# Kernel optimization log

Measured on AMD Instinct MI355X. Metric: run time of the kernel, lower is better.

Reference implementation:

```python
import jax, jax.numpy as jnp
import numpy as np

B, T = 64, 512
OBS, DM, DS, NL = 115, 128, 8, 3
EMB, NA, H1 = 16, 19, 256


def _ln(x, g, b, eps=1e-5):
    m = jnp.mean(x, -1, keepdims=True)
    v = jnp.mean((x - m) ** 2, -1, keepdims=True)
    return (x - m) * jax.lax.rsqrt(v + eps) * g + b


def _s6(x, h, lng, lnb, w_ig, w_dt, b_dt, a_log, w_b, w_c, d_par, w_out):
    # x: [B,T,DM], h: [B,DM,DS]
    xn = _ln(x, lng, lnb)
    xp = xn @ w_ig.T                               # [B,T,2*DM]
    x_in, z = xp[..., :DM], xp[..., DM:]
    dt = jax.nn.softplus(x_in @ w_dt.T + b_dt)     # [B,T,DM]
    A = -jnp.exp(a_log)                            # [DM,DS]
    bt = x_in @ w_b.T                              # [B,T,DS]
    ct = x_in @ w_c.T                              # [B,T,DS]
    dA = jnp.exp(dt[..., None] * A)                # [B,T,DM,DS]
    upd = (dt * x_in)[..., None] * bt[:, :, None, :]  # [B,T,DM,DS]

    def step(hc, inp):
        dA_t, u_t, c_t = inp
        hn = dA_t * hc + u_t                       # [B,DM,DS]
        y = jnp.einsum('bds,bs->bd', hn, c_t)      # [B,DM]
        return hn, y

    h_f, ys = jax.lax.scan(
        step, h,
        (jnp.swapaxes(dA, 0, 1), jnp.swapaxes(upd, 0, 1), jnp.swapaxes(ct, 0, 1)))
    y = jnp.swapaxes(ys, 0, 1)                     # [B,T,DM]
    ssm = y * jax.nn.silu(z) + x_in * d_par
    return x + ssm @ w_out.T, h_f.reshape(h_f.shape[0], -1)


def _forward(prev_actions, obs, h0, enc_w1, enc_b1, enc_g1, enc_bb1, enc_w2, enc_b2,
             enc_g2, enc_bb2, emb, proj_w, proj_b, proj_g, proj_bb,
             m_ln_g, m_ln_b, m_w_ig, m_w_dt, m_b_dt, m_a_log, m_w_b, m_w_c, m_d, m_w_out,
             fn_g, fn_b, pol_w1, pol_b1, pol_g, pol_bb, pol_w2, pol_b2):
    # MLP encoder: Linear -> LN -> SiLU -> Linear -> LN (final norm)
    e = jax.nn.silu(_ln(obs @ enc_w1.T + enc_b1, enc_g1, enc_bb1))
    e = _ln(e @ enc_w2.T + enc_b2, enc_g2, enc_bb2)
    pa = emb[prev_actions]                         # [B,T,EMB]
    x = jnp.concatenate([e, pa], -1) @ proj_w.T + proj_b
    x = jax.nn.silu(_ln(x, proj_g, proj_bb))
    for i in range(NL):
        x, _ = _s6(x, h0[i].reshape(-1, DM, DS), m_ln_g[i], m_ln_b[i], m_w_ig[i],
                   m_w_dt[i], m_b_dt[i], m_a_log[i], m_w_b[i], m_w_c[i], m_d[i], m_w_out[i])
    x = _ln(x, fn_g, fn_b)
    p = jax.nn.silu(_ln(x @ pol_w1.T + pol_b1, pol_g, pol_bb))
    return p @ pol_w2.T + pol_b2                   # [B,T,NA] policy logits


def setup_inputs() -> dict:
    key = jax.random.key(0)
    ks = iter(jax.random.split(key, 64))
    def n(shape, s=0.05):
        return jax.random.normal(next(ks), shape, dtype=jnp.float32) * s
    return {
        'obs': jax.random.normal(next(ks), (B, T, OBS), dtype=jnp.float32),
        'h0': jnp.zeros((NL, B, DM * DS), jnp.float32),
        'enc_w1': n((H1, OBS)), 'enc_b1': jnp.zeros((H1,)),
        'enc_g1': jnp.ones((H1,)), 'enc_bb1': jnp.zeros((H1,)),
        'enc_w2': n((DM, H1)), 'enc_b2': jnp.zeros((DM,)),
        'enc_g2': jnp.ones((DM,)), 'enc_bb2': jnp.zeros((DM,)),
        'emb': n((NA + 1, EMB), 1.0),
        'proj_w': n((DM, DM + EMB)), 'proj_b': jnp.zeros((DM,)),
        'proj_g': jnp.ones((DM,)), 'proj_bb': jnp.zeros((DM,)),
        'm_ln_g': jnp.ones((NL, DM)), 'm_ln_b': jnp.zeros((NL, DM)),
        'm_w_ig': n((NL, 2 * DM, DM)), 'm_w_dt': n((NL, DM, DM)),
        'm_b_dt': jnp.zeros((NL, DM)),
        'm_a_log': jax.random.uniform(next(ks), (NL, DM, DS), minval=-3.0, maxval=-1.0, dtype=jnp.float32),
        'm_w_b': n((NL, DS, DM)), 'm_w_c': n((NL, DS, DM)),
        'm_d': jnp.ones((NL, DM)), 'm_w_out': n((NL, DM, DM)),
        'fn_g': jnp.ones((DM,)), 'fn_b': jnp.zeros((DM,)),
        'pol_w1': n((DM, DM)), 'pol_b1': jnp.zeros((DM,)),
        'pol_g': jnp.ones((DM,)), 'pol_bb': jnp.zeros((DM,)),
        'pol_w2': n((NA, DM)), 'pol_b2': jnp.zeros((NA,)),
        'prev_actions': jax.random.randint(next(ks), (B, T), 0, NA + 1),
    }


def reference(obs, h0, enc_w1, enc_b1, enc_g1, enc_bb1, enc_w2, enc_b2, enc_g2, enc_bb2,
              emb, proj_w, proj_b, proj_g, proj_bb, m_ln_g, m_ln_b, m_w_ig, m_w_dt,
              m_b_dt, m_a_log, m_w_b, m_w_c, m_d, m_w_out, fn_g, fn_b, pol_w1, pol_b1,
              pol_g, pol_bb, pol_w2, pol_b2, prev_actions):
    return _forward(prev_actions, obs, h0, enc_w1, enc_b1, enc_g1, enc_bb1, enc_w2,
                    enc_b2, enc_g2, enc_bb2, emb, proj_w, proj_b, proj_g, proj_bb,
                    m_ln_g, m_ln_b, m_w_ig, m_w_dt, m_b_dt, m_a_log, m_w_b, m_w_c,
                    m_d, m_w_out, fn_g, fn_b, pol_w1, pol_b1, pol_g, pol_bb, pol_w2, pol_b2)
```

## Files before the change

### kernel.cpp

```cpp
#include <hip/hip_runtime.h>
#include <math.h>

#define BB 64
#define TT 512
#define OBSD 115
#define DMD 128
#define DSD 8
#define NLD 3
#define EMBD 16
#define NAD 19
#define H1D 256
#define NTOK (BB*TT)
#define SSEG 32
#define TSEG (TT/SSEG)

typedef unsigned short ushort_t;
typedef __attribute__((ext_vector_type(8))) short short8;
typedef __attribute__((ext_vector_type(4))) float f32x4;

__device__ __forceinline__ float silu_f(float x){ return x / (1.f + __expf(-x)); }
__device__ __forceinline__ float softplus_f(float x){
  return fmaxf(x, 0.f) + log1pf(__expf(-fabsf(x)));
}
__device__ __forceinline__ ushort_t f2bf(float x){
  unsigned u = __float_as_uint(x);
  unsigned r = (u + 0x7fffu + ((u >> 16) & 1u)) >> 16;
  return (ushort_t)r;
}
__device__ __forceinline__ float b2f(ushort_t x){
  return __uint_as_float(((unsigned)x) << 16);
}
#define MFMA(a,b,c) __builtin_amdgcn_mfma_f32_16x16x32_bf16((a),(b),(c),0,0,0)
#define LOG2E 1.44269504f

struct PJob { const float* src; ushort_t* dst; int N; int K; int Kpad; int rowofs; int Nw; };
struct PJobs { PJob j[20]; };

__global__ __launch_bounds__(256) void k_prep(PJobs P){
  const int job = blockIdx.x >> 2;
  const int sub = blockIdx.x & 3;
  PJob pj = P.j[job];
  const int elems = pj.Nw * pj.Kpad;
  for (int idx = sub*256 + threadIdx.x; idx < elems; idx += 4*256){
    int n = idx / pj.Kpad;
    int k = idx - n*pj.Kpad;
    float v = (n < pj.N && k < pj.K) ? pj.src[(size_t)n*pj.K + k] : 0.f;
    pj.dst[(size_t)(pj.rowofs + n)*pj.Kpad + k] = f2bf(v);
  }
}

__global__ __launch_bounds__(256, 4) void k_enc12p(
    const float* __restrict__ obs, const ushort_t* __restrict__ w1b,
    const float* __restrict__ b1, const float* __restrict__ g1,
    const float* __restrict__ bb1,
    const ushort_t* __restrict__ w2b,
    const float* __restrict__ b2, const float* __restrict__ g2,
    const float* __restrict__ bb2,
    const float* __restrict__ emb, const int* __restrict__ pact,
    const ushort_t* __restrict__ pwb, const float* __restrict__ pb,
    const float* __restrict__ pg, const float* __restrict__ pbb,
    float* __restrict__ X,
    const float* __restrict__ lng, const float* __restrict__ lnb,
    const ushort_t* __restrict__ wigb, const ushort_t* __restrict__ wdbcb,
    const float* __restrict__ bdt,
    ushort_t* __restrict__ XINb, ushort_t* __restrict__ Zb,
    ushort_t* __restrict__ DTb, ushort_t* __restrict__ BTu, ushort_t* __restrict__ CTu,
    const float* __restrict__ alog0,
    float* __restrict__ HLOC, float* __restrict__ PPR)
{
  __shared__ __align__(16) char sm[29184];
  ushort_t* s_obs  = (ushort_t*)sm;
  ushort_t* s_e1   = (ushort_t*)sm;
  ushort_t* s_xin  = (ushort_t*)sm;
  ushort_t* s_dt   = (ushort_t*)(sm + 8704);
  ushort_t* s_a2   = (ushort_t*)(sm + 16896);
  ushort_t* s_btc  = (ushort_t*)(sm + 27648);
  float2*   s_st   = (float2*)(sm + 28160);
  float2*   s_st2  = (float2*)(sm + 28672);

  const int tok0 = blockIdx.x * 32;
  const int bidx = blockIdx.x >> 4;
  const int ch   = blockIdx.x & 15;
  const int tid = threadIdx.x;
  const int lane = tid & 63, w = tid >> 6;
  const int q = lane >> 4, cn = lane & 15;
  const int m0 = (w & 1) * 16, nh = w >> 1;

  for (int e = tid; e < 32*16; e += 256){
    int t = e >> 4, kc = e & 15;
    const float* op = obs + (size_t)(tok0 + t)*OBSD;
    short8 v;
    #pragma unroll
    for (int j = 0; j < 8; j++){
      int k = kc*8 + j;
      v[j] = (short)f2bf(k < OBSD ? op[k] : 0.f);
    }
    *(short8*)&s_obs[t*136 + kc*8] = v;
  }
  for (int e = tid; e < 32*32; e += 256){
    int t = e >> 5, k = e & 31;
    float v = 0.f;
    if (k < EMBD){ int a = pact[tok0 + t]; v = emb[(size_t)a*EMBD + k]; }
    s_a2[t*168 + 128 + k] = f2bf(v);
  }
  __syncthreads();

  f32x4 acc[8];
  {
    short8 af[4];
    #pragma unroll
    for (int ks = 0; ks < 4; ks++)
      af[ks] = *(const short8*)&s_obs[(m0 + cn)*136 + ks*32 + q*8];
    #pragma unroll
    for (int nt = 0; nt < 8; nt++){
      const int n0 = (nh*8 + nt) * 16;
      f32x4 a = {0.f,0.f,0.f,0.f};
      #pragma unroll
      for (int ks = 0; ks < 4; ks++){
        short8 bf = *(const short8*)&w1b[(size_t)(n0 + cn)*128 + ks*32 + q*8];
        a = MFMA(af[ks], bf, a);
      }
      float bv = b1[n0 + cn];
      #pragma unroll
      for (int r = 0; r < 4; r++) a[r] += bv;
      acc[nt] = a;
    }
    #pragma unroll
    for (int r = 0; r < 4; r++){
      float s = 0.f, s2 = 0.f;
      #pragma unroll
      for (int nt = 0; nt < 8; nt++){ float v = acc[nt][r]; s += v; s2 = fmaf(v, v, s2); }
      s += __shfl_xor(s, 1, 64); s2 += __shfl_xor(s2, 1, 64);
      s += __shfl_xor(s, 2, 64); s2 += __shfl_xor(s2, 2, 64);
      s += __shfl_xor(s, 4, 64); s2 += __shfl_xor(s2, 4, 64);
      s += __shfl_xor(s, 8, 64); s2 += __shfl_xor(s2, 8, 64);
      if (cn == 0) s_st[(m0 + q*4 + r)*2 + nh] = make_float2(s, s2);
    }
  }
  __syncthreads();

  {
    float mu[4], rs[4];
    #pragma unroll
    for (int r = 0; r < 4; r++){
      const int row = m0 + q*4 + r;
      float2 p0 = s_st[row*2 + 0], p1 = s_st[row*2 + 1];
      float s = p0.x + p1.x, s2 = p0.y + p1.y;
      float m = s * (1.f/256.f);
      mu[r] = m;
      rs[r] = rsqrtf(s2 * (1.f/256.f) - m*m + 1e-5f);
    }
    #pragma unroll
    for (int nt = 0; nt < 8; nt++){
      const int col = (nh*8 + nt)*16 + cn;
      float gg = g1[col], bbv = bb1[col];
      #pragma unroll
      for (int r = 0; r < 4; r++){
        float v = (acc[nt][r] - mu[r]) * rs[r] * gg + bbv;
        s_e1[(m0 + q*4 + r)*264 + col] = f2bf(silu_f(v));
      }
    }
  }
  __syncthreads();

  f32x4 acc2[4];
  {
    short8 af2[8];
    #pragma unroll
    for (int ks = 0; ks < 8; ks++)
      af2[ks] = *(const short8*)&s_e1[(m0 + cn)*264 + ks*32 + q*8];
    #pragma unroll
    for (int nt = 0; nt < 4; nt++){
      const int n0 = (nh*4 + nt) * 16;
      f32x4 a = {0.f,0.f,0.f,0.f};
      #pragma unroll
      for (int ks = 0; ks < 8; ks++){
        short8 bf = *(const short8*)&w2b[(size_t)(n0 + cn)*256 + ks*32 + q*8];
        a = MFMA(af2[ks], bf, a);
      }
      float bv = b2[n0 + cn];
      #pragma unroll
      for (int r = 0; r < 4; r++) a[r] += bv;
      acc2[nt] = a;
    }
    #pragma unroll
    for (int r = 0; r < 4; r++){
      float s = 0.f, s2 = 0.f;
      #pragma unroll
      for (int nt = 0; nt < 4; nt++){ float v = acc2[nt][r]; s += v; s2 = fmaf(v, v, s2); }
      s += __shfl_xor(s, 1, 64); s2 += __shfl_xor(s2, 1, 64);
      s += __shfl_xor(s, 2, 64); s2 += __shfl_xor(s2, 2, 64);
      s += __shfl_xor(s, 4, 64); s2 += __shfl_xor(s2, 4, 64);
      s += __shfl_xor(s, 8, 64); s2 += __shfl_xor(s2, 8, 64);
      if (cn == 0) s_st[(m0 + q*4 + r)*2 + nh] = make_float2(s, s2);
    }
  }
  __syncthreads();

  {
    float mu[4], rs[4];
    #pragma unroll
    for (int r = 0; r < 4; r++){
      const int row = m0 + q*4 + r;
      float2 p0 = s_st[row*2 + 0], p1 = s_st[row*2 + 1];
      float s = p0.x + p1.x, s2 = p0.y + p1.y;
      float m = s * (1.f/128.f);
      mu[r] = m;
      rs[r] = rsqrtf(s2 * (1.f/128.f) - m*m + 1e-5f);
    }
    #pragma unroll
    for (int nt = 0; nt < 4; nt++){
      const int col = (nh*4 + nt)*16 + cn;
      float gg = g2[col], bbv = bb2[col];
      #pragma unroll
      for (int r = 0; r < 4; r++){
        float v = (acc2[nt][r] - mu[r]) * rs[r] * gg + bbv;
        s_a2[(m0 + q*4 + r)*168 + col] = f2bf(v);
      }
    }
  }
  __syncthreads();

  f32x4 acc3[4];
  {
    short8 af3[5];
    #pragma unroll
    for (int ks = 0; ks < 5; ks++)
      af3[ks] = *(const short8*)&s_a2[(m0 + cn)*168 + ks*32 + q*8];
    #pragma unroll
    for (int nt = 0; nt < 4; nt++){
      const int n0 = (nh*4 + nt) * 16;
      f32x4 a = {0.f,0.f,0.f,0.f};
      #pragma unroll
      for (int ks = 0; ks < 5; ks++){
        short8 bf = *(const short8*)&pwb[(size_t)(n0 + cn)*160 + ks*32 + q*8];
        a = MFMA(af3[ks], bf, a);
      }
      float bv = pb[n0 + cn];
      #pragma unroll
      for (int r = 0; r < 4; r++) a[r] += bv;
      acc3[nt] = a;
    }
    #pragma unroll
    for (int r = 0; r < 4; r++){
      float s = 0.f, s2 = 0.f;
      #pragma unroll
      for (int nt = 0; nt < 4; nt++){ float v = acc3[nt][r]; s += v; s2 = fmaf(v, v, s2); }
      s += __shfl_xor(s, 1, 64); s2 += __shfl_xor(s2, 1, 64);
      s += __shfl_xor(s, 2, 64); s2 += __shfl_xor(s2, 2, 64);
      s += __shfl_xor(s, 4, 64); s2 += __shfl_xor(s2, 4, 64);
      s += __shfl_xor(s, 8, 64); s2 += __shfl_xor(s2, 8, 64);
      if (cn == 0) s_st[(m0 + q*4 + r)*2 + nh] = make_float2(s, s2);
    }
  }
  __syncthreads();

  {
    float mu[4], rs[4];
    #pragma unroll
    for (int r = 0; r < 4; r++){
      const int row = m0 + q*4 + r;
      float2 p0 = s_st[row*2 + 0], p1 = s_st[row*2 + 1];
      float s = p0.x + p1.x, s2 = p0.y + p1.y;
      float m = s * (1.f/128.f);
      mu[r] = m;
      rs[r] = rsqrtf(s2 * (1.f/128.f) - m*m + 1e-5f);
    }
    float ps[4] = {0.f,0.f,0.f,0.f}, ps2[4] = {0.f,0.f,0.f,0.f};
    #pragma unroll
    for (int nt = 0; nt < 4; nt++){
      const int col = (nh*4 + nt)*16 + cn;
      float gg = pg[col], bbv = pbb[col];
      #pragma unroll
      for (int r = 0; r < 4; r++){
        float v = (acc3[nt][r] - mu[r]) * rs[r] * gg + bbv;
        v = silu_f(v);
        acc3[nt][r] = v;
        X[(size_t)(tok0 + m0 + q*4 + r)*128 + col] = v;
        ps[r] += v; ps2[r] = fmaf(v, v, ps2[r]);
      }
    }
    #pragma unroll
    for (int r = 0; r < 4; r++){
      float s = ps[r], s2 = ps2[r];
      s += __shfl_xor(s, 1, 64); s2 += __shfl_xor(s2, 1, 64);
      s += __shfl_xor(s, 2, 64); s2 += __shfl_xor(s2, 2, 64);
      s += __shfl_xor(s, 4, 64); s2 += __shfl_xor(s2, 4, 64);
      s += __shfl_xor(s, 8, 64); s2 += __shfl_xor(s2, 8, 64);
      if (cn == 0) s_st2[(m0 + q*4 + r)*2 + nh] = make_float2(s, s2);
    }
  }
  __syncthreads();

  {
    float mu[4], rs[4];
    #pragma unroll
    for (int r = 0; r < 4; r++){
      const int row = m0 + q*4 + r;
      float2 p0 = s_st2[row*2 + 0], p1 = s_st2[row*2 + 1];
      float s = p0.x + p1.x, s2 = p0.y + p1.y;
      float m = s * (1.f/128.f);
      mu[r] = m;
      rs[r] = rsqrtf(s2 * (1.f/128.f) - m*m + 1e-5f);
    }
    #pragma unroll
    for (int nt = 0; nt < 4; nt++){
      const int col = (nh*4 + nt)*16 + cn;
      float gg = lng[col], bbv = lnb[col];
      #pragma unroll
      for (int r = 0; r < 4; r++){
        float v = (acc3[nt][r] - mu[r]) * rs[r] * gg + bbv;
        s_a2[(m0 + q*4 + r)*168 + col] = f2bf(v);
      }
    }
  }
  __syncthreads();

  {
    short8 af[4];
    #pragma unroll
    for (int ks = 0; ks < 4; ks++)
      af[ks] = *(const short8*)&s_a2[(m0 + cn)*168 + ks*32 + q*8];
    #pragma unroll
    for (int nt = 0; nt < 8; nt++){
      const int n0 = (nh*8 + nt) * 16;
      f32x4 a = {0.f,0.f,0.f,0.f};
      #pragma unroll
      for (int ks = 0; ks < 4; ks++){
        short8 bf = *(const short8*)&wigb[(size_t)(n0 + cn)*128 + ks*32 + q*8];
        a = MFMA(af[ks], bf, a);
      }
      if (n0 < 128){
        #pragma unroll
        for (int r = 0; r < 4; r++){
          int tr = m0 + q*4 + r;
          ushort_t bb = f2bf(a[r]);
          XINb[(size_t)(tok0 + tr)*128 + n0 + cn] = bb;
          s_xin[tr*136 + n0 + cn] = bb;
        }
      } else {
        #pragma unroll
        for (int r = 0; r < 4; r++){
          int tr = m0 + q*4 + r;
          Zb[(size_t)(tok0 + tr)*128 + (n0 - 128) + cn] = f2bf(a[r]);
        }
      }
    }
  }
  __syncthreads();

  {
    short8 af2[4];
    #pragma unroll
    for (int ks = 0; ks < 4; ks++)
      af2[ks] = *(const short8*)&s_xin[(m0 + cn)*136 + ks*32 + q*8];
    for (int nt = nh; nt < 9; nt += 2){
      const int n0 = nt * 16;
      f32x4 a = {0.f,0.f,0.f,0.f};
      #pragma unroll
      for (int ks = 0; ks < 4; ks++){
        short8 bf = *(const short8*)&wdbcb[(size_t)(n0 + cn)*128 + ks*32 + q*8];
        a = MFMA(af2[ks], bf, a);
      }
      const int col = n0 + cn;
      if (col < 128){
        float bd = bdt[col];
        #pragma unroll
        for (int r = 0; r < 4; r++){
          int tr = m0 + q*4 + r;
          ushort_t dv = f2bf(softplus_f(a[r] + bd));
          DTb[(size_t)(tok0 + tr)*128 + col] = dv;
          s_dt[tr*136 + col] = dv;
        }
      } else if (col < 136){
        #pragma unroll
        for (int r = 0; r < 4; r++){
          int tr = m0 + q*4 + r;
          ushort_t bb = f2bf(a[r]);
          BTu[(size_t)(tok0 + tr)*8 + (col - 128)] = bb;
          s_btc[tr*8 + (col - 128)] = bb;
        }
      } else {
        #pragma unroll
        for (int r = 0; r < 4; r++)
          CTu[(size_t)(tok0 + m0 + q*4 + r)*8 + (col - 136)] = f2bf(a[r]);
      }
    }
  }
  __syncthreads();

  {
    const int d = tid & 127, half = tid >> 7;
    float A2c[8], hh[8], pp[8];
    #pragma unroll
    for (int s = 0; s < 8; s++){
      A2c[s] = -__expf(alog0[d*8 + s]) * LOG2E;
      hh[s] = 0.f; pp[s] = 1.f;
    }
    const int t0 = half * 16;
    #pragma unroll 4
    for (int tt = 0; tt < 16; tt++){
      const int t = t0 + tt;
      float dt = b2f(s_dt[t*136 + d]);
      float wv = dt * b2f(s_xin[t*136 + d]);
      #pragma unroll
      for (int s = 0; s < 8; s++){
        float dA = exp2f(dt * A2c[s]);
        hh[s] = fmaf(dA, hh[s], wv * b2f(s_btc[t*8 + s]));
        pp[s] *= dA;
      }
    }
    const size_t o = ((size_t)bidx*SSEG + ch*2 + half)*1024 + d*8;
    #pragma unroll
    for (int s = 0; s < 8; s++){ HLOC[o+s] = hh[s]; PPR[o+s] = pp[s]; }
  }
}

__global__ __launch_bounds__(256) void k_carry(
    float* __restrict__ HL, const float* __restrict__ PP,
    const float* __restrict__ h0g)
{
  const int idx = blockIdx.x*256 + threadIdx.x;
  const size_t base = (size_t)(idx >> 10) * (SSEG*1024) + (idx & 1023);
  float hl[SSEG], pp[SSEG];
  #pragma unroll
  for (int ch = 0; ch < SSEG; ch++){
    hl[ch] = HL[base + (size_t)ch*1024];
    pp[ch] = PP[base + (size_t)ch*1024];
  }
  float h = h0g[idx];
  #pragma unroll
  for (int ch = 0; ch < SSEG; ch++){
    HL[base + (size_t)ch*1024] = h;
    h = fmaf(pp[ch], h, hl[ch]);
  }
}

#define SMB 34816

__device__ __forceinline__ void phaseB32(
    const ushort_t* DTb, const ushort_t* XINb, const ushort_t* Zb,
    const ushort_t* BTu, const ushort_t* CTu,
    const float* __restrict__ alog, const float* __restrict__ HLpre,
    const float* __restrict__ dpar, const ushort_t* __restrict__ woutb,
    float* __restrict__ X, char* sm, int b, int pair, int tid)
{
  ushort_t* s_dtS = (ushort_t*)sm;
  ushort_t* s_xiS = (ushort_t*)(sm + 8192);
  ushort_t* s_zS  = (ushort_t*)(sm + 16384);
  float*    s_x   = (float*)sm;
  ushort_t* s_a   = (ushort_t*)(sm + 24576);
  ushort_t* s_bt  = (ushort_t*)(sm + 33280);
  ushort_t* s_ct  = (ushort_t*)(sm + 33792);
  float2*   s_st  = (float2*)(sm + 34304);

  const int lane = tid & 63, w = tid >> 6, q = lane >> 4, cn = lane & 15;
  const int m0 = (w & 1) * 16, nh = w >> 1;
  const int d = tid & 127, half = tid >> 7;
  const size_t segtok = (size_t)b*TT + pair*32;

  {
    const uint4* gdt = (const uint4*)(DTb + segtok*128);
    const uint4* gxi = (const uint4*)(XINb + segtok*128);
    const uint4* gz  = (const uint4*)(Zb + segtok*128);
    #pragma unroll
    for (int i = 0; i < 2; i++){
      ((uint4*)s_dtS)[tid + i*256] = gdt[tid + i*256];
      ((uint4*)s_xiS)[tid + i*256] = gxi[tid + i*256];
      ((uint4*)s_zS )[tid + i*256] = gz [tid + i*256];
    }
    if (tid < 128){
      ((unsigned*)s_bt)[tid] = ((const unsigned*)(BTu + segtok*8))[tid];
      ((unsigned*)s_ct)[tid] = ((const unsigned*)(CTu + segtok*8))[tid];
    }
  }
  float A2[8], h[8];
  float dp = dpar[d];
  {
    const size_t o = ((size_t)b*SSEG + pair*2 + half)*1024 + d*8;
    float4 h0v = *(const float4*)(HLpre + o);
    float4 h1v = *(const float4*)(HLpre + o + 4);
    h[0]=h0v.x; h[1]=h0v.y; h[2]=h0v.z; h[3]=h0v.w;
    h[4]=h1v.x; h[5]=h1v.y; h[6]=h1v.z; h[7]=h1v.w;
    #pragma unroll
    for (int s = 0; s < 8; s++) A2[s] = -__expf(alog[d*8 + s]) * LOG2E;
  }
  __syncthreads();

  #pragma unroll 4
  for (int tt = 0; tt < 16; tt++){
    const int t = half*16 + tt;
    float dt = b2f(s_dtS[t*128 + d]);
    float xi = b2f(s_xiS[t*128 + d]);
    float zv = b2f(s_zS [t*128 + d]);
    float wv = dt * xi;
    float y = 0.f;
    #pragma unroll
    for (int s = 0; s < 8; s++){
      float dA = exp2f(dt * A2[s]);
      h[s] = fmaf(dA, h[s], wv * b2f(s_bt[t*8 + s]));
      y = fmaf(h[s], b2f(s_ct[t*8 + s]), y);
    }
    float ssm = y * silu_f(zv) + xi * dp;
    s_a[t*136 + d] = f2bf(ssm);
  }
  __syncthreads();

  {
    short8 af[4];
    #pragma unroll
    for (int ks = 0; ks < 4; ks++)
      af[ks] = *(const short8*)&s_a[(m0 + cn)*136 + ks*32 + q*8];
    float ps[4] = {0.f,0.f,0.f,0.f}, ps2[4] = {0.f,0.f,0.f,0.f};
    #pragma unroll
    for (int i = 0; i < 4; i++){
      const int n0 = (nh*4 + i) * 16;
      short8 bf[4];
      #pragma unroll
      for (int ks = 0; ks < 4; ks++)
        bf[ks] = *(const short8*)&woutb[(size_t)(n0+cn)*128 + ks*32 + q*8];
      f32x4 acc = {0.f,0.f,0.f,0.f};
      #pragma unroll
      for (int ks = 0; ks < 4; ks++) acc = MFMA(af[ks], bf[ks], acc);
      #pragma unroll
      for (int r = 0; r < 4; r++){
        const int tr = m0 + q*4 + r;
        const size_t g = (segtok + tr)*128 + n0 + cn;
        float xn = X[g] + acc[r];
        X[g] = xn;
        s_x[tr*130 + n0 + cn] = xn;
        ps[r] += xn; ps2[r] = fmaf(xn, xn, ps2[r]);
      }
    }
    #pragma unroll
    for (int r = 0; r < 4; r++){
      float s = ps[r], s2 = ps2[r];
      s += __shfl_xor(s, 1, 64); s2 += __shfl_xor(s2, 1, 64);
      s += __shfl_xor(s, 2, 64); s2 += __shfl_xor(s2, 2, 64);
      s += __shfl_xor(s, 4, 64); s2 += __shfl_xor(s2, 4, 64);
      s += __shfl_xor(s, 8, 64); s2 += __shfl_xor(s2, 8, 64);
      if (cn == 0) s_st[(m0 + q*4 + r)*2 + nh] = make_float2(s, s2);
    }
  }
  __syncthreads();
}

__global__ __launch_bounds__(256, 4) void k_scan2p(
    ushort_t* DTb, ushort_t* XINb, ushort_t* Zb,
    ushort_t* BTu, ushort_t* CTu,
    const float* __restrict__ alog, const float* __restrict__ HLpre,
    const float* __restrict__ dpar, const ushort_t* __restrict__ woutb,
    float* __restrict__ X,
    const float* __restrict__ lng, const float* __restrict__ lnb,
    const ushort_t* __restrict__ wigb, const ushort_t* __restrict__ wdbcb,
    const float* __restrict__ bdt,
    const float* __restrict__ alogn,
    float* __restrict__ HLo, float* __restrict__ PPo)
{
  __shared__ __align__(16) char sm[SMB];
  const int tid = threadIdx.x;
  float*    s_x   = (float*)sm;
  ushort_t* s_xin = (ushort_t*)sm;
  ushort_t* s_dt2 = (ushort_t*)(sm + 8704);
  ushort_t* s_a   = (ushort_t*)(sm + 24576);
  ushort_t* s_btc = (ushort_t*)(sm + 33280);
  float2*   s_st  = (float2*)(sm + 34304);

  const int b = blockIdx.x >> 4;
  const int pair = blockIdx.x & 15;
  const int lane = tid & 63, w = tid >> 6, q = lane >> 4, cn = lane & 15;
  const int m0 = (w & 1) * 16, nh = w >> 1;
  const int d = tid & 127, half = tid >> 7;
  const size_t segtok = (size_t)b*TT + pair*32;

  phaseB32(DTb, XINb, Zb, BTu, CTu, alog, HLpre, dpar, woutb, X, sm, b, pair, tid);

  {
    float g = lng[d], c0v = lnb[d];
    #pragma unroll
    for (int tt = 0; tt < 16; tt++){
      const int t = half*16 + tt;
      float2 p0 = s_st[t*2 + 0], p1 = s_st[t*2 + 1];
      float ssum = p0.x + p1.x, ss2 = p0.y + p1.y;
      float mu = ssum * (1.f/128.f);
      float rs = rsqrtf(ss2 * (1.f/128.f) - mu*mu + 1e-5f);
      float v = (s_x[t*130 + d] - mu) * rs * g + c0v;
      s_a[t*136 + d] = f2bf(v);
    }
  }
  __syncthreads();

  {
    short8 af[4];
    #pragma unroll
    for (int ks = 0; ks < 4; ks++)
      af[ks] = *(const short8*)&s_a[(m0 + cn)*136 + ks*32 + q*8];
    #pragma unroll
    for (int i = 0; i < 8; i++){
      const int n0 = (nh*8 + i) * 16;
      short8 bf[4];
      #pragma unroll
      for (int ks = 0; ks < 4; ks++)
        bf[ks] = *(const short8*)&wigb[(size_t)(n0+cn)*128 + ks*32 + q*8];
      f32x4 acc = {0.f,0.f,0.f,0.f};
      #pragma unroll
      for (int ks = 0; ks < 4; ks++) acc = MFMA(af[ks], bf[ks], acc);
      if (n0 < 128){
        #pragma unroll
        for (int r = 0; r < 4; r++){
          const int tr = m0 + q*4 + r;
          ushort_t bb = f2bf(acc[r]);
          XINb[(segtok + tr)*128 + n0 + cn] = bb;
          s_xin[tr*136 + n0 + cn] = bb;
        }
      } else {
        #pragma unroll
        for (int r = 0; r < 4; r++){
          const int tr = m0 + q*4 + r;
          Zb[(segtok + tr)*128 + (n0-128) + cn] = f2bf(acc[r]);
        }
      }
    }
  }
  __syncthreads();

  {
    short8 af2[4];
    #pragma unroll
    for (int ks = 0; ks < 4; ks++)
      af2[ks] = *(const short8*)&s_xin[(m0 + cn)*136 + ks*32 + q*8];
    for (int nt = nh; nt < 9; nt += 2){
      const int n0 = nt * 16;
      short8 bf[4];
      #pragma unroll
      for (int ks = 0; ks < 4; ks++)
        bf[ks] = *(const short8*)&wdbcb[(size_t)(n0+cn)*128 + ks*32 + q*8];
      f32x4 acc = {0.f,0.f,0.f,0.f};
      #pragma unroll
      for (int ks = 0; ks < 4; ks++) acc = MFMA(af2[ks], bf[ks], acc);
      const int col = n0 + cn;
      if (col < 128){
        float bd = bdt[col];
        #pragma unroll
        for (int r = 0; r < 4; r++){
          const int tr = m0 + q*4 + r;
          ushort_t dv = f2bf(softplus_f(acc[r] + bd));
          DTb[(segtok + tr)*128 + col] = dv;
          s_dt2[tr*136 + col] = dv;
        }
      } else if (col < 136){
        #pragma unroll
        for (int r = 0; r < 4; r++){
          const int tr = m0 + q*4 + r;
          ushort_t bb = f2bf(acc[r]);
          BTu[(segtok + tr)*8 + (col-128)] = bb;
          s_btc[tr*8 + (col-128)] = bb;
        }
      } else {
        #pragma unroll
        for (int r = 0; r < 4; r++)
          CTu[(segtok + m0 + q*4 + r)*8 + (col-136)] = f2bf(acc[r]);
      }
    }
  }
  __syncthreads();

  {
    float A2n[8], hh[8], pp[8];
    #pragma unroll
    for (int s = 0; s < 8; s++){
      A2n[s] = -__expf(alogn[d*8 + s]) * LOG2E;
      hh[s] = 0.f; pp[s] = 1.f;
    }
    #pragma unroll 4
    for (int tt = 0; tt < 16; tt++){
      const int t = half*16 + tt;
      float dt = b2f(s_dt2[t*136 + d]);
      float wv = dt * b2f(s_xin[t*136 + d]);
      #pragma unroll
      for (int s = 0; s < 8; s++){
        float dA = exp2f(dt * A2n[s]);
        hh[s] = fmaf(dA, hh[s], wv * b2f(s_btc[t*8 + s]));
        pp[s] *= dA;
      }
    }
    const size_t o = ((size_t)b*SSEG + pair*2 + half)*1024 + d*8;
    #pragma unroll
    for (int s = 0; s < 8; s++){ HLo[o+s] = hh[s]; PPo[o+s] = pp[s]; }
  }
}

__global__ __launch_bounds__(256, 4) void k_scan2h(
    const ushort_t* DTb, const ushort_t* XINb, const ushort_t* Zb,
    const ushort_t* BTu, const ushort_t* CTu,
    const float* __restrict__ alog, const float* __restrict__ HLpre,
    const float* __restrict__ dpar, const ushort_t* __restrict__ woutb,
    float* __restrict__ X,
    const float* __restrict__ fng, const float* __restrict__ fnb,
    const ushort_t* __restrict__ pw1b, const float* __restrict__ pb1,
    const float* __restrict__ pg, const float* __restrict__ pbb,
    const ushort_t* __restrict__ pw2b, const float* __restrict__ pb2,
    float* __restrict__ out)
{
  __shared__ __align__(16) char sm[SMB];
  const int tid = threadIdx.x;
  float*    s_x  = (float*)sm;
  ushort_t* s_a  = (ushort_t*)(sm + 24576);
  float2*   s_st = (float2*)(sm + 34304);

  const int b = blockIdx.x >> 4;
  const int pair = blockIdx.x & 15;
  const int lane = tid & 63, w = tid >> 6, q = lane >> 4, cn = lane & 15;
  const int m0 = (w & 1) * 16, nh = w >> 1;
  const int d = tid & 127, half = tid >> 7;
  const size_t segtok = (size_t)b*TT + pair*32;

  phaseB32((ushort_t*)DTb, (ushort_t*)XINb, (ushort_t*)Zb,
           (ushort_t*)BTu, (ushort_t*)CTu, alog, HLpre,
           dpar, woutb, X, sm, b, pair, tid);

  {
    float g = fng[d], c0v = fnb[d];
    #pragma unroll
    for (int tt = 0; tt < 16; tt++){
      const int t = half*16 + tt;
      float2 p0 = s_st[t*2 + 0], p1 = s_st[t*2 + 1];
      float ssum = p0.x + p1.x, ss2 = p0.y + p1.y;
      float mu = ssum * (1.f/128.f);
      float rs = rsqrtf(ss2 * (1.f/128.f) - mu*mu + 1e-5f);
      float v = (s_x[t*130 + d] - mu) * rs * g + c0v;
      s_a[t*136 + d] = f2bf(v);
    }
  }
  __syncthreads();

  {
    short8 af[4];
    #pragma unroll
    for (int ks = 0; ks < 4; ks++)
      af[ks] = *(const short8*)&s_a[(m0 + cn)*136 + ks*32 + q*8];
    float ps[4] = {0.f,0.f,0.f,0.f}, ps2[4] = {0.f,0.f,0.f,0.f};
    #pragma unroll
    for (int i = 0; i < 4; i++){
      const int n0 = (nh*4 + i) * 16;
      short8 bf[4];
      #pragma unroll
      for (int ks = 0; ks < 4; ks++)
        bf[ks] = *(const short8*)&pw1b[(size_t)(n0+cn)*128 + ks*32 + q*8];
      float bias = pb1[n0 + cn];
      f32x4 acc = {0.f,0.f,0.f,0.f};
      #pragma unroll
      for (int ks = 0; ks < 4; ks++) acc = MFMA(af[ks], bf[ks], acc);
      #pragma unroll
      for (int r = 0; r < 4; r++){
        float xv = acc[r] + bias;
        s_x[(m0 + q*4 + r)*130 + n0 + cn] = xv;
        ps[r] += xv; ps2[r] = fmaf(xv, xv, ps2[r]);
      }
    }
    #pragma unroll
    for (int r = 0; r < 4; r++){
      float s = ps[r], s2 = ps2[r];
      s += __shfl_xor(s, 1, 64); s2 += __shfl_xor(s2, 1, 64);
      s += __shfl_xor(s, 2, 64); s2 += __shfl_xor(s2, 2, 64);
      s += __shfl_xor(s, 4, 64); s2 += __shfl_xor(s2, 4, 64);
      s += __shfl_xor(s, 8, 64); s2 += __shfl_xor(s2, 8, 64);
      if (cn == 0) s_st[(m0 + q*4 + r)*2 + nh] = make_float2(s, s2);
    }
  }
  __syncthreads();

  {
    float g = pg[d], c0v = pbb[d];
    #pragma unroll
    for (int tt = 0; tt < 16; tt++){
      const int t = half*16 + tt;
      float2 p0 = s_st[t*2 + 0], p1 = s_st[t*2 + 1];
      float ssum = p0.x + p1.x, ss2 = p0.y + p1.y;
      float mu = ssum * (1.f/128.f);
      float rs = rsqrtf(ss2 * (1.f/128.f) - mu*mu + 1e-5f);
      float v = (s_x[t*130 + d] - mu) * rs * g + c0v;
      s_a[t*136 + d] = f2bf(silu_f(v));
    }
  }
  __syncthreads();

  {
    short8 af[4];
    #pragma unroll
    for (int ks = 0; ks < 4; ks++)
      af[ks] = *(const short8*)&s_a[(m0 + cn)*136 + ks*32 + q*8];
    const int n0 = (w >> 1) * 16;
    short8 bf[4];
    #pragma unroll
    for (int ks = 0; ks < 4; ks++)
      bf[ks] = *(const short8*)&pw2b[(size_t)(n0+cn)*128 + ks*32 + q*8];
    const int col = n0 + cn;
    f32x4 acc = {0.f,0.f,0.f,0.f};
    #pragma unroll
    for (int ks = 0; ks < 4; ks++) acc = MFMA(af[ks], bf[ks], acc);
    if (col < NAD){
      float bias = pb2[col];
      #pragma unroll
      for (int r = 0; r < 4; r++)
        out[(segtok + m0 + q*4 + r)*NAD + col] = acc[r] + bias;
    }
  }
}

extern "C" void kernel_launch(void* const* d_in, const int* in_sizes, int n_in,
                              void* d_out, int out_size, void* d_ws, size_t ws_size,
                              hipStream_t stream) {
  const float* obs    = (const float*)d_in[0];
  const float* h0     = (const float*)d_in[1];
  const float* enc_w1 = (const float*)d_in[2];
  const float* enc_b1 = (const float*)d_in[3];
  const float* enc_g1 = (const float*)d_in[4];
  const float* enc_bb1= (const float*)d_in[5];
  const float* enc_w2 = (const float*)d_in[6];
  const float* enc_b2 = (const float*)d_in[7];
  const float* enc_g2 = (const float*)d_in[8];
  const float* enc_bb2= (const float*)d_in[9];
  const float* emb    = (const float*)d_in[10];
  const float* proj_w = (const float*)d_in[11];
  const float* proj_b = (const float*)d_in[12];
  const float* proj_g = (const float*)d_in[13];
  const float* proj_bb= (const float*)d_in[14];
  const float* m_ln_g = (const float*)d_in[15];
  const float* m_ln_b = (const float*)d_in[16];
  const float* m_w_ig = (const float*)d_in[17];
  const float* m_w_dt = (const float*)d_in[18];
  const float* m_b_dt = (const float*)d_in[19];
  const float* m_a_log= (const float*)d_in[20];
  const float* m_w_b  = (const float*)d_in[21];
  const float* m_w_c  = (const float*)d_in[22];
  const float* m_d    = (const float*)d_in[23];
  const float* m_w_out= (const float*)d_in[24];
  const float* fn_g   = (const float*)d_in[25];
  const float* fn_b   = (const float*)d_in[26];
  const float* pol_w1 = (const float*)d_in[27];
  const float* pol_b1 = (const float*)d_in[28];
  const float* pol_g  = (const float*)d_in[29];
  const float* pol_bb = (const float*)d_in[30];
  const float* pol_w2 = (const float*)d_in[31];
  const float* pol_b2 = (const float*)d_in[32];
  const int*   pact   = (const int*)d_in[33];

  float* ws  = (float*)d_ws;
  float* X    = ws;
  float* HLA  = X + (size_t)NTOK*128;
  float* PPA  = HLA + (size_t)BB*SSEG*1024;
  float* HLB  = PPA + (size_t)BB*SSEG*1024;
  float* PPB  = HLB + (size_t)BB*SSEG*1024;
  ushort_t* XINb = (ushort_t*)(PPB + (size_t)BB*SSEG*1024);
  ushort_t* Zb   = XINb + (size_t)NTOK*128;
  ushort_t* DTb  = Zb   + (size_t)NTOK*128;
  ushort_t* BTu  = DTb  + (size_t)NTOK*128;
  ushort_t* CTu  = BTu  + (size_t)NTOK*8;

  ushort_t* W1B   = CTu   + (size_t)NTOK*8;
  ushort_t* W2B   = W1B   + 256*128;
  ushort_t* PWB   = W2B   + 128*256;
  ushort_t* WIGB  = PWB   + 128*160;
  ushort_t* WDBCB = WIGB  + 3*256*128;
  ushort_t* WOUTB = WDBCB + 3*144*128;
  ushort_t* PW1B  = WOUTB + 3*128*128;
  ushort_t* PW2B  = PW1B  + 128*128;

  PJobs P;
  int nj = 0;
  auto add = [&](const float* src, ushort_t* dst, int N, int K, int Kpad, int rowofs, int Nw){
    P.j[nj].src = src; P.j[nj].dst = dst; P.j[nj].N = N; P.j[nj].K = K;
    P.j[nj].Kpad = Kpad; P.j[nj].rowofs = rowofs; P.j[nj].Nw = Nw; nj++;
  };
  add(enc_w1, W1B, 256, 115, 128, 0, 256);
  add(enc_w2, W2B, 128, 256, 256, 0, 128);
  add(proj_w, PWB, 128, 144, 160, 0, 128);
  for (int l = 0; l < NLD; l++)
    add(m_w_ig + (size_t)l*256*128, WIGB + (size_t)l*256*128, 256, 128, 128, 0, 256);
  for (int l = 0; l < NLD; l++){
    add(m_w_dt + (size_t)l*128*128, WDBCB + (size_t)l*144*128, 128, 128, 128, 0,   128);
    add(m_w_b  + (size_t)l*8*128,   WDBCB + (size_t)l*144*128,   8, 128, 128, 128,   8);
    add(m_w_c  + (size_t)l*8*128,   WDBCB + (size_t)l*144*128,   8, 128, 128, 136,   8);
  }
  for (int l = 0; l < NLD; l++)
    add(m_w_out + (size_t)l*128*128, WOUTB + (size_t)l*128*128, 128, 128, 128, 0, 128);
  add(pol_w1, PW1B, 128, 128, 128, 0, 128);
  add(pol_w2, PW2B,  19, 128, 128, 0,  32);

  k_prep<<<20*4, 256, 0, stream>>>(P);
  k_enc12p<<<NTOK/32, 256, 0, stream>>>(obs, W1B, enc_b1, enc_g1, enc_bb1,
      W2B, enc_b2, enc_g2, enc_bb2,
      emb, pact, PWB, proj_b, proj_g, proj_bb, X,
      m_ln_g, m_ln_b, WIGB, WDBCB, m_b_dt,
      XINb, Zb, DTb, BTu, CTu,
      m_a_log, HLA, PPA);

  const int carrygrid = BB*1024/256;
  const int scangrid  = NTOK/32;

  k_carry<<<carrygrid, 256, 0, stream>>>(HLA, PPA, h0);
  k_scan2p<<<scangrid, 256, 0, stream>>>(DTb, XINb, Zb, BTu, CTu,
      m_a_log, HLA, m_d, WOUTB, X,
      m_ln_g + 128, m_ln_b + 128,
      WIGB + (size_t)256*128, WDBCB + (size_t)144*128, m_b_dt + 128,
      m_a_log + 1024, HLB, PPB);
  k_carry<<<carrygrid, 256, 0, stream>>>(HLB, PPB, h0 + (size_t)BB*1024);
  k_scan2p<<<scangrid, 256, 0, stream>>>(DTb, XINb, Zb, BTu, CTu,
      m_a_log + 1024, HLB, m_d + 128, WOUTB + (size_t)128*128, X,
      m_ln_g + 256, m_ln_b + 256,
      WIGB + (size_t)2*256*128, WDBCB + (size_t)2*144*128, m_b_dt + 256,
      m_a_log + 2048, HLA, PPA);
  k_carry<<<carrygrid, 256, 0, stream>>>(HLA, PPA, h0 + (size_t)2*BB*1024);
  k_scan2h<<<scangrid, 256, 0, stream>>>(DTb, XINb, Zb, BTu, CTu,
      m_a_log + 2048, HLA, m_d + 256, WOUTB + (size_t)2*128*128, X,
      fn_g, fn_b, PW1B, pol_b1, pol_g, pol_bb, PW2B, pol_b2,
      (float*)d_out);
}
```

Measured before the change: 407.0 us.

## Halve per-block token tile to 16 and split scan state across threads

Each block in the encoder and scan kernels now processes 16 tokens instead of 32, which doubles the grid and roughly halves LDS per block. The four waves split the N dimension of every GEMM instead of splitting M and N in a 2x2 arrangement. In the local scan, the two thread halves each take four of the eight state channels rather than half of the time steps. Launch bounds are raised to allow more blocks per CU. The aim is better occupancy and latency hiding, at the cost of weight fragments being reloaded once per 16 tokens instead of once per 32.

```diff
diff --git a/kernel.cpp b/kernel.cpp
--- a/kernel.cpp
+++ b/kernel.cpp
@@ -49,7 +49,7 @@
   }
 }
 
-__global__ __launch_bounds__(256, 4) void k_enc12p(
+__global__ __launch_bounds__(256, 8) void k_enc12p(
     const float* __restrict__ obs, const ushort_t* __restrict__ w1b,
     const float* __restrict__ b1, const float* __restrict__ g1,
     const float* __restrict__ bb1,
@@ -68,26 +68,25 @@
     const float* __restrict__ alog0,
     float* __restrict__ HLOC, float* __restrict__ PPR)
 {
-  __shared__ __align__(16) char sm[29184];
-  ushort_t* s_obs  = (ushort_t*)sm;
-  ushort_t* s_e1   = (ushort_t*)sm;
-  ushort_t* s_xin  = (ushort_t*)sm;
-  ushort_t* s_dt   = (ushort_t*)(sm + 8704);
-  ushort_t* s_a2   = (ushort_t*)(sm + 16896);
-  ushort_t* s_btc  = (ushort_t*)(sm + 27648);
-  float2*   s_st   = (float2*)(sm + 28160);
-  float2*   s_st2  = (float2*)(sm + 28672);
-
-  const int tok0 = blockIdx.x * 32;
-  const int bidx = blockIdx.x >> 4;
-  const int ch   = blockIdx.x & 15;
+  __shared__ __align__(16) char sm[15104];
+  ushort_t* s_obs = (ushort_t*)sm;
+  ushort_t* s_e1  = (ushort_t*)sm;
+  ushort_t* s_xin = (ushort_t*)sm;
+  ushort_t* s_dt  = (ushort_t*)(sm + 4352);
+  ushort_t* s_a2  = (ushort_t*)(sm + 8448);
+  ushort_t* s_btc = (ushort_t*)(sm + 13824);
+  float2*   s_st  = (float2*)(sm + 14080);
+  float2*   s_st2 = (float2*)(sm + 14592);
+
+  const int tok0 = blockIdx.x * 16;
+  const int bidx = blockIdx.x >> 5;
+  const int ch   = blockIdx.x & 31;
   const int tid = threadIdx.x;
   const int lane = tid & 63, w = tid >> 6;
   const int q = lane >> 4, cn = lane & 15;
-  const int m0 = (w & 1) * 16, nh = w >> 1;
-
-  for (int e = tid; e < 32*16; e += 256){
-    int t = e >> 4, kc = e & 15;
+
+  {
+    const int t = tid >> 4, kc = tid & 15;
     const float* op = obs + (size_t)(tok0 + t)*OBSD;
     short8 v;
     #pragma unroll
@@ -97,7 +96,7 @@
     }
     *(short8*)&s_obs[t*136 + kc*8] = v;
   }
-  for (int e = tid; e < 32*32; e += 256){
+  for (int e = tid; e < 16*32; e += 256){
     int t = e >> 5, k = e & 31;
     float v = 0.f;
     if (k < EMBD){ int a = pact[tok0 + t]; v = emb[(size_t)a*EMBD + k]; }
@@ -105,15 +104,15 @@
   }
   __syncthreads();
 
-  f32x4 acc[8];
+  f32x4 acc[4];
   {
     short8 af[4];
     #pragma unroll
     for (int ks = 0; ks < 4; ks++)
-      af[ks] = *(const short8*)&s_obs[(m0 + cn)*136 + ks*32 + q*8];
-    #pragma unroll
-    for (int nt = 0; nt < 8; nt++){
-      const int n0 = (nh*8 + nt) * 16;
+      af[ks] = *(const short8*)&s_obs[cn*136 + ks*32 + q*8];
+    #pragma unroll
+    for (int nt = 0; nt < 4; nt++){
+      const int n0 = (w*4 + nt) * 16;
       f32x4 a = {0.f,0.f,0.f,0.f};
       #pragma unroll
       for (int ks = 0; ks < 4; ks++){
@@ -129,12 +128,12 @@
     for (int r = 0; r < 4; r++){
       float s = 0.f, s2 = 0.f;
       #pragma unroll
-      for (int nt = 0; nt < 8; nt++){ float v = acc[nt][r]; s += v; s2 = fmaf(v, v, s2); }
+      for (int nt = 0; nt < 4; nt++){ float v = acc[nt][r]; s += v; s2 = fmaf(v, v, s2); }
       s += __shfl_xor(s, 1, 64); s2 += __shfl_xor(s2, 1, 64);
       s += __shfl_xor(s, 2, 64); s2 += __shfl_xor(s2, 2, 64);
       s += __shfl_xor(s, 4, 64); s2 += __shfl_xor(s2, 4, 64);
       s += __shfl_xor(s, 8, 64); s2 += __shfl_xor(s2, 8, 64);
-      if (cn == 0) s_st[(m0 + q*4 + r)*2 + nh] = make_float2(s, s2);
+      if (cn == 0) s_st[(q*4 + r)*4 + w] = make_float2(s, s2);
     }
   }
   __syncthreads();
@@ -143,35 +142,36 @@
     float mu[4], rs[4];
     #pragma unroll
     for (int r = 0; r < 4; r++){
-      const int row = m0 + q*4 + r;
-      float2 p0 = s_st[row*2 + 0], p1 = s_st[row*2 + 1];
-      float s = p0.x + p1.x, s2 = p0.y + p1.y;
+      const int row = q*4 + r;
+      float2 p0 = s_st[row*4+0], p1 = s_st[row*4+1];
+      float2 p2 = s_st[row*4+2], p3 = s_st[row*4+3];
+      float s = p0.x+p1.x+p2.x+p3.x, s2 = p0.y+p1.y+p2.y+p3.y;
       float m = s * (1.f/256.f);
       mu[r] = m;
       rs[r] = rsqrtf(s2 * (1.f/256.f) - m*m + 1e-5f);
     }
     #pragma unroll
-    for (int nt = 0; nt < 8; nt++){
-      const int col = (nh*8 + nt)*16 + cn;
+    for (int nt = 0; nt < 4; nt++){
+      const int col = (w*4 + nt)*16 + cn;
       float gg = g1[col], bbv = bb1[col];
       #pragma unroll
       for (int r = 0; r < 4; r++){
         float v = (acc[nt][r] - mu[r]) * rs[r] * gg + bbv;
-        s_e1[(m0 + q*4 + r)*264 + col] = f2bf(silu_f(v));
-      }
-    }
-  }
-  __syncthreads();
-
-  f32x4 acc2[4];
+        s_e1[(q*4 + r)*264 + col] = f2bf(silu_f(v));
+      }
+    }
+  }
+  __syncthreads();
+
+  f32x4 acc2[2];
   {
     short8 af2[8];
     #pragma unroll
     for (int ks = 0; ks < 8; ks++)
-      af2[ks] = *(const short8*)&s_e1[(m0 + cn)*264 + ks*32 + q*8];
-    #pragma unroll
-    for (int nt = 0; nt < 4; nt++){
-      const int n0 = (nh*4 + nt) * 16;
+      af2[ks] = *(const short8*)&s_e1[cn*264 + ks*32 + q*8];
+    #pragma unroll
+    for (int nt = 0; nt < 2; nt++){
+      const int n0 = (w*2 + nt) * 16;
       f32x4 a = {0.f,0.f,0.f,0.f};
       #pragma unroll
       for (int ks = 0; ks < 8; ks++){
@@ -187,12 +187,12 @@
     for (int r = 0; r < 4; r++){
       float s = 0.f, s2 = 0.f;
       #pragma unroll
-      for (int nt = 0; nt < 4; nt++){ float v = acc2[nt][r]; s += v; s2 = fmaf(v, v, s2); }
+      for (int nt = 0; nt < 2; nt++){ float v = acc2[nt][r]; s += v; s2 = fmaf(v, v, s2); }
       s += __shfl_xor(s, 1, 64); s2 += __shfl_xor(s2, 1, 64);
       s += __shfl_xor(s, 2, 64); s2 += __shfl_xor(s2, 2, 64);
       s += __shfl_xor(s, 4, 64); s2 += __shfl_xor(s2, 4, 64);
       s += __shfl_xor(s, 8, 64); s2 += __shfl_xor(s2, 8, 64);
-      if (cn == 0) s_st[(m0 + q*4 + r)*2 + nh] = make_float2(s, s2);
+      if (cn == 0) s_st[(q*4 + r)*4 + w] = make_float2(s, s2);
     }
   }
   __syncthreads();
@@ -201,35 +201,36 @@
     float mu[4], rs[4];
     #pragma unroll
     for (int r = 0; r < 4; r++){
-      const int row = m0 + q*4 + r;
-      float2 p0 = s_st[row*2 + 0], p1 = s_st[row*2 + 1];
-      float s = p0.x + p1.x, s2 = p0.y + p1.y;
+      const int row = q*4 + r;
+      float2 p0 = s_st[row*4+0], p1 = s_st[row*4+1];
+      float2 p2 = s_st[row*4+2], p3 = s_st[row*4+3];
+      float s = p0.x+p1.x+p2.x+p3.x, s2 = p0.y+p1.y+p2.y+p3.y;
       float m = s * (1.f/128.f);
       mu[r] = m;
       rs[r] = rsqrtf(s2 * (1.f/128.f) - m*m + 1e-5f);
     }
     #pragma unroll
-    for (int nt = 0; nt < 4; nt++){
-      const int col = (nh*4 + nt)*16 + cn;
+    for (int nt = 0; nt < 2; nt++){
+      const int col = (w*2 + nt)*16 + cn;
       float gg = g2[col], bbv = bb2[col];
       #pragma unroll
       for (int r = 0; r < 4; r++){
         float v = (acc2[nt][r] - mu[r]) * rs[r] * gg + bbv;
-        s_a2[(m0 + q*4 + r)*168 + col] = f2bf(v);
-      }
-    }
-  }
-  __syncthreads();
-
-  f32x4 acc3[4];
+        s_a2[(q*4 + r)*168 + col] = f2bf(v);
+      }
+    }
+  }
+  __syncthreads();
+
+  f32x4 acc3[2];
   {
     short8 af3[5];
     #pragma unroll
     for (int ks = 0; ks < 5; ks++)
-      af3[ks] = *(const short8*)&s_a2[(m0 + cn)*168 + ks*32 + q*8];
-    #pragma unroll
-    for (int nt = 0; nt < 4; nt++){
-      const int n0 = (nh*4 + nt) * 16;
+      af3[ks] = *(const short8*)&s_a2[cn*168 + ks*32 + q*8];
+    #pragma unroll
+    for (int nt = 0; nt < 2; nt++){
+      const int n0 = (w*2 + nt) * 16;
       f32x4 a = {0.f,0.f,0.f,0.f};
       #pragma unroll
       for (int ks = 0; ks < 5; ks++){
@@ -245,12 +246,12 @@
     for (int r = 0; r < 4; r++){
       float s = 0.f, s2 = 0.f;
       #pragma unroll
-      for (int nt = 0; nt < 4; nt++){ float v = acc3[nt][r]; s += v; s2 = fmaf(v, v, s2); }
+      for (int nt = 0; nt < 2; nt++){ float v = acc3[nt][r]; s += v; s2 = fmaf(v, v, s2); }
       s += __shfl_xor(s, 1, 64); s2 += __shfl_xor(s2, 1, 64);
       s += __shfl_xor(s, 2, 64); s2 += __shfl_xor(s2, 2, 64);
       s += __shfl_xor(s, 4, 64); s2 += __shfl_xor(s2, 4, 64);
       s += __shfl_xor(s, 8, 64); s2 += __shfl_xor(s2, 8, 64);
-      if (cn == 0) s_st[(m0 + q*4 + r)*2 + nh] = make_float2(s, s2);
+      if (cn == 0) s_st[(q*4 + r)*4 + w] = make_float2(s, s2);
     }
   }
   __syncthreads();
@@ -259,24 +260,25 @@
     float mu[4], rs[4];
     #pragma unroll
     for (int r = 0; r < 4; r++){
-      const int row = m0 + q*4 + r;
-      float2 p0 = s_st[row*2 + 0], p1 = s_st[row*2 + 1];
-      float s = p0.x + p1.x, s2 = p0.y + p1.y;
+      const int row = q*4 + r;
+      float2 p0 = s_st[row*4+0], p1 = s_st[row*4+1];
+      float2 p2 = s_st[row*4+2], p3 = s_st[row*4+3];
+      float s = p0.x+p1.x+p2.x+p3.x, s2 = p0.y+p1.y+p2.y+p3.y;
       float m = s * (1.f/128.f);
       mu[r] = m;
       rs[r] = rsqrtf(s2 * (1.f/128.f) - m*m + 1e-5f);
     }
     float ps[4] = {0.f,0.f,0.f,0.f}, ps2[4] = {0.f,0.f,0.f,0.f};
     #pragma unroll
-    for (int nt = 0; nt < 4; nt++){
-      const int col = (nh*4 + nt)*16 + cn;
+    for (int nt = 0; nt < 2; nt++){
+      const int col = (w*2 + nt)*16 + cn;
       float gg = pg[col], bbv = pbb[col];
       #pragma unroll
       for (int r = 0; r < 4; r++){
         float v = (acc3[nt][r] - mu[r]) * rs[r] * gg + bbv;
         v = silu_f(v);
         acc3[nt][r] = v;
-        X[(size_t)(tok0 + m0 + q*4 + r)*128 + col] = v;
+        X[(size_t)(tok0 + q*4 + r)*128 + col] = v;
         ps[r] += v; ps2[r] = fmaf(v, v, ps2[r]);
       }
     }
@@ -287,7 +289,7 @@
       s += __shfl_xor(s, 2, 64); s2 += __shfl_xor(s2, 2, 64);
       s += __shfl_xor(s, 4, 64); s2 += __shfl_xor(s2, 4, 64);
       s += __shfl_xor(s, 8, 64); s2 += __shfl_xor(s2, 8, 64);
-      if (cn == 0) s_st2[(m0 + q*4 + r)*2 + nh] = make_float2(s, s2);
+      if (cn == 0) s_st2[(q*4 + r)*4 + w] = make_float2(s, s2);
     }
   }
   __syncthreads();
@@ -296,21 +298,22 @@
     float mu[4], rs[4];
     #pragma unroll
     for (int r = 0; r < 4; r++){
-      const int row = m0 + q*4 + r;
-      float2 p0 = s_st2[row*2 + 0], p1 = s_st2[row*2 + 1];
-      float s = p0.x + p1.x, s2 = p0.y + p1.y;
+      const int row = q*4 + r;
+      float2 p0 = s_st2[row*4+0], p1 = s_st2[row*4+1];
+      float2 p2 = s_st2[row*4+2], p3 = s_st2[row*4+3];
+      float s = p0.x+p1.x+p2.x+p3.x, s2 = p0.y+p1.y+p2.y+p3.y;
       float m = s * (1.f/128.f);
       mu[r] = m;
       rs[r] = rsqrtf(s2 * (1.f/128.f) - m*m + 1e-5f);
     }
     #pragma unroll
-    for (int nt = 0; nt < 4; nt++){
-      const int col = (nh*4 + nt)*16 + cn;
+    for (int nt = 0; nt < 2; nt++){
+      const int col = (w*2 + nt)*16 + cn;
       float gg = lng[col], bbv = lnb[col];
       #pragma unroll
       for (int r = 0; r < 4; r++){
         float v = (acc3[nt][r] - mu[r]) * rs[r] * gg + bbv;
-        s_a2[(m0 + q*4 + r)*168 + col] = f2bf(v);
+        s_a2[(q*4 + r)*168 + col] = f2bf(v);
       }
     }
   }
@@ -320,10 +323,10 @@
     short8 af[4];
     #pragma unroll
     for (int ks = 0; ks < 4; ks++)
-      af[ks] = *(const short8*)&s_a2[(m0 + cn)*168 + ks*32 + q*8];
-    #pragma unroll
-    for (int nt = 0; nt < 8; nt++){
-      const int n0 = (nh*8 + nt) * 16;
+      af[ks] = *(const short8*)&s_a2[cn*168 + ks*32 + q*8];
+    #pragma unroll
+    for (int i = 0; i < 4; i++){
+      const int n0 = (w*4 + i) * 16;
       f32x4 a = {0.f,0.f,0.f,0.f};
       #pragma unroll
       for (int ks = 0; ks < 4; ks++){
@@ -333,7 +336,7 @@
       if (n0 < 128){
         #pragma unroll
         for (int r = 0; r < 4; r++){
-          int tr = m0 + q*4 + r;
+          int tr = q*4 + r;
           ushort_t bb = f2bf(a[r]);
           XINb[(size_t)(tok0 + tr)*128 + n0 + cn] = bb;
           s_xin[tr*136 + n0 + cn] = bb;
@@ -341,7 +344,7 @@
       } else {
         #pragma unroll
         for (int r = 0; r < 4; r++){
-          int tr = m0 + q*4 + r;
+          int tr = q*4 + r;
           Zb[(size_t)(tok0 + tr)*128 + (n0 - 128) + cn] = f2bf(a[r]);
         }
       }
@@ -353,8 +356,8 @@
     short8 af2[4];
     #pragma unroll
     for (int ks = 0; ks < 4; ks++)
-      af2[ks] = *(const short8*)&s_xin[(m0 + cn)*136 + ks*32 + q*8];
-    for (int nt = nh; nt < 9; nt += 2){
+      af2[ks] = *(const short8*)&s_xin[cn*136 + ks*32 + q*8];
+    for (int nt = w; nt < 9; nt += 4){
       const int n0 = nt * 16;
       f32x4 a = {0.f,0.f,0.f,0.f};
       #pragma unroll
@@ -367,7 +370,7 @@
         float bd = bdt[col];
         #pragma unroll
         for (int r = 0; r < 4; r++){
-          int tr = m0 + q*4 + r;
+          int tr = q*4 + r;
           ushort_t dv = f2bf(softplus_f(a[r] + bd));
           DTb[(size_t)(tok0 + tr)*128 + col] = dv;
           s_dt[tr*136 + col] = dv;
@@ -375,7 +378,7 @@
       } else if (col < 136){
         #pragma unroll
         for (int r = 0; r < 4; r++){
-          int tr = m0 + q*4 + r;
+          int tr = q*4 + r;
           ushort_t bb = f2bf(a[r]);
           BTu[(size_t)(tok0 + tr)*8 + (col - 128)] = bb;
           s_btc[tr*8 + (col - 128)] = bb;
@@ -383,36 +386,34 @@
       } else {
         #pragma unroll
         for (int r = 0; r < 4; r++)
-          CTu[(size_t)(tok0 + m0 + q*4 + r)*8 + (col - 136)] = f2bf(a[r]);
-      }
-    }
-  }
-  __syncthreads();
-
-  {
-    const int d = tid & 127, half = tid >> 7;
-    float A2c[8], hh[8], pp[8];
-    #pragma unroll
-    for (int s = 0; s < 8; s++){
-      A2c[s] = -__expf(alog0[d*8 + s]) * LOG2E;
-      hh[s] = 0.f; pp[s] = 1.f;
-    }
-    const int t0 = half * 16;
+          CTu[(size_t)(tok0 + q*4 + r)*8 + (col - 136)] = f2bf(a[r]);
+      }
+    }
+  }
+  __syncthreads();
+
+  {
+    const int d = tid & 127, sh = tid >> 7;
+    float A2c[4], hh[4], pp[4];
+    #pragma unroll
+    for (int j = 0; j < 4; j++){
+      A2c[j] = -__expf(alog0[d*8 + sh*4 + j]) * LOG2E;
+      hh[j] = 0.f; pp[j] = 1.f;
+    }
     #pragma unroll 4
-    for (int tt = 0; tt < 16; tt++){
-      const int t = t0 + tt;
+    for (int t = 0; t < 16; t++){
       float dt = b2f(s_dt[t*136 + d]);
       float wv = dt * b2f(s_xin[t*136 + d]);
       #pragma unroll
-      for (int s = 0; s < 8; s++){
-        float dA = exp2f(dt * A2c[s]);
-        hh[s] = fmaf(dA, hh[s], wv * b2f(s_btc[t*8 + s]));
-        pp[s] *= dA;
-      }
-    }
-    const size_t o = ((size_t)bidx*SSEG + ch*2 + half)*1024 + d*8;
-    #pragma unroll
-    for (int s = 0; s < 8; s++){ HLOC[o+s] = hh[s]; PPR[o+s] = pp[s]; }
+      for (int j = 0; j < 4; j++){
+        float dA = exp2f(dt * A2c[j]);
+        hh[j] = fmaf(dA, hh[j], wv * b2f(s_btc[t*8 + sh*4 + j]));
+        pp[j] *= dA;
+      }
+    }
+    const size_t o = ((size_t)bidx*SSEG + ch)*1024 + d*8 + sh*4;
+    #pragma unroll
+    for (int j = 0; j < 4; j++){ HLOC[o+j] = hh[j]; PPR[o+j] = pp[j]; }
   }
 }
 
@@ -436,73 +437,66 @@
   }
 }
 
-#define SMB 34816
-
-__device__ __forceinline__ void phaseB32(
+#define SMB 17664
+
+__device__ __forceinline__ void phaseB16(
     const ushort_t* DTb, const ushort_t* XINb, const ushort_t* Zb,
     const ushort_t* BTu, const ushort_t* CTu,
     const float* __restrict__ alog, const float* __restrict__ HLpre,
     const float* __restrict__ dpar, const ushort_t* __restrict__ woutb,
-    float* __restrict__ X, char* sm, int b, int pair, int tid)
+    float* __restrict__ X, char* sm, int b, int seg, int tid)
 {
   ushort_t* s_dtS = (ushort_t*)sm;
-  ushort_t* s_xiS = (ushort_t*)(sm + 8192);
-  ushort_t* s_zS  = (ushort_t*)(sm + 16384);
+  ushort_t* s_xiS = (ushort_t*)(sm + 4096);
+  ushort_t* s_zS  = (ushort_t*)(sm + 8192);
   float*    s_x   = (float*)sm;
-  ushort_t* s_a   = (ushort_t*)(sm + 24576);
-  ushort_t* s_bt  = (ushort_t*)(sm + 33280);
-  ushort_t* s_ct  = (ushort_t*)(sm + 33792);
-  float2*   s_st  = (float2*)(sm + 34304);
+  ushort_t* s_a   = (ushort_t*)(sm + 12288);
+  ushort_t* s_bt  = (ushort_t*)(sm + 16640);
+  ushort_t* s_ct  = (ushort_t*)(sm + 16896);
+  float2*   s_st  = (float2*)(sm + 17152);
 
   const int lane = tid & 63, w = tid >> 6, q = lane >> 4, cn = lane & 15;
-  const int m0 = (w & 1) * 16, nh = w >> 1;
-  const int d = tid & 127, half = tid >> 7;
-  const size_t segtok = (size_t)b*TT + pair*32;
-
-  {
-    const uint4* gdt = (const uint4*)(DTb + segtok*128);
-    const uint4* gxi = (const uint4*)(XINb + segtok*128);
-    const uint4* gz  = (const uint4*)(Zb + segtok*128);
-    #pragma unroll
-    for (int i = 0; i < 2; i++){
-      ((uint4*)s_dtS)[tid + i*256] = gdt[tid + i*256];
-      ((uint4*)s_xiS)[tid + i*256] = gxi[tid + i*256];
-      ((uint4*)s_zS )[tid + i*256] = gz [tid + i*256];
-    }
-    if (tid < 128){
-      ((unsigned*)s_bt)[tid] = ((const unsigned*)(BTu + segtok*8))[tid];
-      ((unsigned*)s_ct)[tid] = ((const unsigned*)(CTu + segtok*8))[tid];
-    }
-  }
-  float A2[8], h[8];
-  float dp = dpar[d];
-  {
-    const size_t o = ((size_t)b*SSEG + pair*2 + half)*1024 + d*8;
+  const size_t segtok = (size_t)b*TT + seg*TSEG;
+
+  ((uint4*)s_dtS)[tid] = ((const uint4*)(DTb  + segtok*128))[tid];
+  ((uint4*)s_xiS)[tid] = ((const uint4*)(XINb + segtok*128))[tid];
+  ((uint4*)s_zS )[tid] = ((const uint4*)(Zb   + segtok*128))[tid];
+  if (tid < 64){
+    ((unsigned*)s_bt)[tid] = ((const unsigned*)(BTu + segtok*8))[tid];
+    ((unsigned*)s_ct)[tid] = ((const unsigned*)(CTu + segtok*8))[tid];
+  }
+  float A2[8], h[8], dp = 0.f;
+  if (tid < 128){
+    const int d = tid;
+    const size_t o = ((size_t)b*SSEG + seg)*1024 + d*8;
     float4 h0v = *(const float4*)(HLpre + o);
     float4 h1v = *(const float4*)(HLpre + o + 4);
     h[0]=h0v.x; h[1]=h0v.y; h[2]=h0v.z; h[3]=h0v.w;
     h[4]=h1v.x; h[5]=h1v.y; h[6]=h1v.z; h[7]=h1v.w;
+    dp = dpar[d];
     #pragma unroll
     for (int s = 0; s < 8; s++) A2[s] = -__expf(alog[d*8 + s]) * LOG2E;
   }
   __syncthreads();
 
-  #pragma unroll 4
-  for (int tt = 0; tt < 16; tt++){
-    const int t = half*16 + tt;
-    float dt = b2f(s_dtS[t*128 + d]);
-    float xi = b2f(s_xiS[t*128 + d]);
-    float zv = b2f(s_zS [t*128 + d]);
-    float wv = dt * xi;
-    float y = 0.f;
-    #pragma unroll
-    for (int s = 0; s < 8; s++){
-      float dA = exp2f(dt * A2[s]);
-      h[s] = fmaf(dA, h[s], wv * b2f(s_bt[t*8 + s]));
-      y = fmaf(h[s], b2f(s_ct[t*8 + s]), y);
-    }
-    float ssm = y * silu_f(zv) + xi * dp;
-    s_a[t*136 + d] = f2bf(ssm);
+  if (tid < 128){
+    const int d = tid;
+    #pragma unroll 4
+    for (int t = 0; t < 16; t++){
+      float dt = b2f(s_dtS[t*128 + d]);
+      float xi = b2f(s_xiS[t*128 + d]);
+      float zv = b2f(s_zS [t*128 + d]);
+      float wv = dt * xi;
+      float y = 0.f;
+      #pragma unroll
+      for (int s = 0; s < 8; s++){
+        float dA = exp2f(dt * A2[s]);
+        h[s] = fmaf(dA, h[s], wv * b2f(s_bt[t*8 + s]));
+        y = fmaf(h[s], b2f(s_ct[t*8 + s]), y);
+      }
+      float ssm = y * silu_f(zv) + xi * dp;
+      s_a[t*136 + d] = f2bf(ssm);
+    }
   }
   __syncthreads();
 
@@ -510,11 +504,11 @@
     short8 af[4];
     #pragma unroll
     for (int ks = 0; ks < 4; ks++)
-      af[ks] = *(const short8*)&s_a[(m0 + cn)*136 + ks*32 + q*8];
+      af[ks] = *(const short8*)&s_a[cn*136 + ks*32 + q*8];
     float ps[4] = {0.f,0.f,0.f,0.f}, ps2[4] = {0.f,0.f,0.f,0.f};
     #pragma unroll
-    for (int i = 0; i < 4; i++){
-      const int n0 = (nh*4 + i) * 16;
+    for (int i = 0; i < 2; i++){
+      const int n0 = (w*2 + i) * 16;
       short8 bf[4];
       #pragma unroll
       for (int ks = 0; ks < 4; ks++)
@@ -524,7 +518,7 @@
       for (int ks = 0; ks < 4; ks++) acc = MFMA(af[ks], bf[ks], acc);
       #pragma unroll
       for (int r = 0; r < 4; r++){
-        const int tr = m0 + q*4 + r;
+        const int tr = q*4 + r;
         const size_t g = (segtok + tr)*128 + n0 + cn;
         float xn = X[g] + acc[r];
         X[g] = xn;
@@ -539,13 +533,13 @@
       s += __shfl_xor(s, 2, 64); s2 += __shfl_xor(s2, 2, 64);
       s += __shfl_xor(s, 4, 64); s2 += __shfl_xor(s2, 4, 64);
       s += __shfl_xor(s, 8, 64); s2 += __shfl_xor(s2, 8, 64);
-      if (cn == 0) s_st[(m0 + q*4 + r)*2 + nh] = make_float2(s, s2);
+      if (cn == 0) s_st[(q*4 + r)*4 + w] = make_float2(s, s2);
     }
   }
   __syncthreads();
 }
 
-__global__ __launch_bounds__(256, 4) void k_scan2p(
+__global__ __launch_bounds__(256, 6) void k_scan2p(
     ushort_t* DTb, ushort_t* XINb, ushort_t* Zb,
     ushort_t* BTu, ushort_t* CTu,
     const float* __restrict__ alog, const float* __restrict__ HLpre,
@@ -561,27 +555,27 @@
   const int tid = threadIdx.x;
   float*    s_x   = (float*)sm;
   ushort_t* s_xin = (ushort_t*)sm;
-  ushort_t* s_dt2 = (ushort_t*)(sm + 8704);
-  ushort_t* s_a   = (ushort_t*)(sm + 24576);
-  ushort_t* s_btc = (ushort_t*)(sm + 33280);
-  float2*   s_st  = (float2*)(sm + 34304);
-
-  const int b = blockIdx.x >> 4;
-  const int pair = blockIdx.x & 15;
+  ushort_t* s_dt2 = (ushort_t*)(sm + 4352);
+  ushort_t* s_a   = (ushort_t*)(sm + 12288);
+  ushort_t* s_btc = (ushort_t*)(sm + 16640);
+  float2*   s_st  = (float2*)(sm + 17152);
+
+  const int b = blockIdx.x >> 5;
+  const int seg = blockIdx.x & 31;
   const int lane = tid & 63, w = tid >> 6, q = lane >> 4, cn = lane & 15;
-  const int m0 = (w & 1) * 16, nh = w >> 1;
-  const int d = tid & 127, half = tid >> 7;
-  const size_t segtok = (size_t)b*TT + pair*32;
-
-  phaseB32(DTb, XINb, Zb, BTu, CTu, alog, HLpre, dpar, woutb, X, sm, b, pair, tid);
-
-  {
+  const size_t segtok = (size_t)b*TT + seg*TSEG;
+
+  phaseB16(DTb, XINb, Zb, BTu, CTu, alog, HLpre, dpar, woutb, X, sm, b, seg, tid);
+
+  {
+    const int d = tid & 127, half = tid >> 7;
     float g = lng[d], c0v = lnb[d];
     #pragma unroll
-    for (int tt = 0; tt < 16; tt++){
-      const int t = half*16 + tt;
-      float2 p0 = s_st[t*2 + 0], p1 = s_st[t*2 + 1];
-      float ssum = p0.x + p1.x, ss2 = p0.y + p1.y;
+    for (int tt = 0; tt < 8; tt++){
+      const int t = half*8 + tt;
+      float2 p0 = s_st[t*4+0], p1 = s_st[t*4+1];
+      float2 p2 = s_st[t*4+2], p3 = s_st[t*4+3];
+      float ssum = p0.x+p1.x+p2.x+p3.x, ss2 = p0.y+p1.y+p2.y+p3.y;
       float mu = ssum * (1.f/128.f);
       float rs = rsqrtf(ss2 * (1.f/128.f) - mu*mu + 1e-5f);
       float v = (s_x[t*130 + d] - mu) * rs * g + c0v;
@@ -594,10 +588,10 @@
     short8 af[4];
     #pragma unroll
     for (int ks = 0; ks < 4; ks++)
-      af[ks] = *(const short8*)&s_a[(m0 + cn)*136 + ks*32 + q*8];
-    #pragma unroll
-    for (int i = 0; i < 8; i++){
-      const int n0 = (nh*8 + i) * 16;
+      af[ks] = *(const short8*)&s_a[cn*136 + ks*32 + q*8];
+    #pragma unroll
+    for (int i = 0; i < 4; i++){
+      const int n0 = (w*4 + i) * 16;
       short8 bf[4];
       #pragma unroll
       for (int ks = 0; ks < 4; ks++)
@@ -608,7 +602,7 @@
       if (n0 < 128){
         #pragma unroll
         for (int r = 0; r < 4; r++){
-          const int tr = m0 + q*4 + r;
+          const int tr = q*4 + r;
           ushort_t bb = f2bf(acc[r]);
           XINb[(segtok + tr)*128 + n0 + cn] = bb;
           s_xin[tr*136 + n0 + cn] = bb;
@@ -616,7 +610,7 @@
       } else {
         #pragma unroll
         for (int r = 0; r < 4; r++){
-          const int tr = m0 + q*4 + r;
+          const int tr = q*4 + r;
           Zb[(segtok + tr)*128 + (n0-128) + cn] = f2bf(acc[r]);
         }
       }
@@ -628,8 +622,8 @@
     short8 af2[4];
     #pragma unroll
     for (int ks = 0; ks < 4; ks++)
-      af2[ks] = *(const short8*)&s_xin[(m0 + cn)*136 + ks*32 + q*8];
-    for (int nt = nh; nt < 9; nt += 2){
+      af2[ks] = *(const short8*)&s_xin[cn*136 + ks*32 + q*8];
+    for (int nt = w; nt < 9; nt += 4){
       const int n0 = nt * 16;
       short8 bf[4];
       #pragma unroll
@@ -643,7 +637,7 @@
         float bd = bdt[col];
         #pragma unroll
         for (int r = 0; r < 4; r++){
-          const int tr = m0 + q*4 + r;
+          const int tr = q*4 + r;
           ushort_t dv = f2bf(softplus_f(acc[r] + bd));
           DTb[(segtok + tr)*128 + col] = dv;
           s_dt2[tr*136 + col] = dv;
@@ -651,7 +645,7 @@
       } else if (col < 136){
         #pragma unroll
         for (int r = 0; r < 4; r++){
-          const int tr = m0 + q*4 + r;
+          const int tr = q*4 + r;
           ushort_t bb = f2bf(acc[r]);
           BTu[(segtok + tr)*8 + (col-128)] = bb;
           s_btc[tr*8 + (col-128)] = bb;
@@ -659,38 +653,38 @@
       } else {
         #pragma unroll
         for (int r = 0; r < 4; r++)
-          CTu[(segtok + m0 + q*4 + r)*8 + (col-136)] = f2bf(acc[r]);
-      }
-    }
-  }
-  __syncthreads();
-
-  {
-    float A2n[8], hh[8], pp[8];
-    #pragma unroll
-    for (int s = 0; s < 8; s++){
-      A2n[s] = -__expf(alogn[d*8 + s]) * LOG2E;
-      hh[s] = 0.f; pp[s] = 1.f;
+          CTu[(segtok + q*4 + r)*8 + (col-136)] = f2bf(acc[r]);
+      }
+    }
+  }
+  __syncthreads();
+
+  {
+    const int d = tid & 127, sh = tid >> 7;
+    float A2n[4], hh[4], pp[4];
+    #pragma unroll
+    for (int j = 0; j < 4; j++){
+      A2n[j] = -__expf(alogn[d*8 + sh*4 + j]) * LOG2E;
+      hh[j] = 0.f; pp[j] = 1.f;
     }
     #pragma unroll 4
-    for (int tt = 0; tt < 16; tt++){
-      const int t = half*16 + tt;
+    for (int t = 0; t < 16; t++){
       float dt = b2f(s_dt2[t*136 + d]);
       float wv = dt * b2f(s_xin[t*136 + d]);
       #pragma unroll
-      for (int s = 0; s < 8; s++){
-        float dA = exp2f(dt * A2n[s]);
-        hh[s] = fmaf(dA, hh[s], wv * b2f(s_btc[t*8 + s]));
-        pp[s] *= dA;
-      }
-    }
-    const size_t o = ((size_t)b*SSEG + pair*2 + half)*1024 + d*8;
-    #pragma unroll
-    for (int s = 0; s < 8; s++){ HLo[o+s] = hh[s]; PPo[o+s] = pp[s]; }
+      for (int j = 0; j < 4; j++){
+        float dA = exp2f(dt * A2n[j]);
+        hh[j] = fmaf(dA, hh[j], wv * b2f(s_btc[t*8 + sh*4 + j]));
+        pp[j] *= dA;
+      }
+    }
+    const size_t o = ((size_t)b*SSEG + seg)*1024 + d*8 + sh*4;
+    #pragma unroll
+    for (int j = 0; j < 4; j++){ HLo[o+j] = hh[j]; PPo[o+j] = pp[j]; }
   }
 }
 
-__global__ __launch_bounds__(256, 4) void k_scan2h(
+__global__ __launch_bounds__(256, 6) void k_scan2h(
     const ushort_t* DTb, const ushort_t* XINb, const ushort_t* Zb,
     const ushort_t* BTu, const ushort_t* CTu,
     const float* __restrict__ alog, const float* __restrict__ HLpre,
@@ -705,27 +699,27 @@
   __shared__ __align__(16) char sm[SMB];
   const int tid = threadIdx.x;
   float*    s_x  = (float*)sm;
-  ushort_t* s_a  = (ushort_t*)(sm + 24576);
-  float2*   s_st = (float2*)(sm + 34304);
-
-  const int b = blockIdx.x >> 4;
-  const int pair = blockIdx.x & 15;
+  ushort_t* s_a  = (ushort_t*)(sm + 12288);
+  float2*   s_st = (float2*)(sm + 17152);
+
+  const int b = blockIdx.x >> 5;
+  const int seg = blockIdx.x & 31;
   const int lane = tid & 63, w = tid >> 6, q = lane >> 4, cn = lane & 15;
-  const int m0 = (w & 1) * 16, nh = w >> 1;
-  const int d = tid & 127, half = tid >> 7;
-  const size_t segtok = (size_t)b*TT + pair*32;
-
-  phaseB32((ushort_t*)DTb, (ushort_t*)XINb, (ushort_t*)Zb,
+  const size_t segtok = (size_t)b*TT + seg*TSEG;
+
+  phaseB16((ushort_t*)DTb, (ushort_t*)XINb, (ushort_t*)Zb,
            (ushort_t*)BTu, (ushort_t*)CTu, alog, HLpre,
-           dpar, woutb, X, sm, b, pair, tid);
-
-  {
+           dpar, woutb, X, sm, b, seg, tid);
+
+  {
+    const int d = tid & 127, half = tid >> 7;
     float g = fng[d], c0v = fnb[d];
     #pragma unroll
-    for (int tt = 0; tt < 16; tt++){
-      const int t = half*16 + tt;
-      float2 p0 = s_st[t*2 + 0], p1 = s_st[t*2 + 1];
-      float ssum = p0.x + p1.x, ss2 = p0.y + p1.y;
+    for (int tt = 0; tt < 8; tt++){
+      const int t = half*8 + tt;
+      float2 p0 = s_st[t*4+0], p1 = s_st[t*4+1];
+      float2 p2 = s_st[t*4+2], p3 = s_st[t*4+3];
+      float ssum = p0.x+p1.x+p2.x+p3.x, ss2 = p0.y+p1.y+p2.y+p3.y;
       float mu = ssum * (1.f/128.f);
       float rs = rsqrtf(ss2 * (1.f/128.f) - mu*mu + 1e-5f);
       float v = (s_x[t*130 + d] - mu) * rs * g + c0v;
@@ -738,11 +732,11 @@
     short8 af[4];
     #pragma unroll
     for (int ks = 0; ks < 4; ks++)
-      af[ks] = *(const short8*)&s_a[(m0 + cn)*136 + ks*32 + q*8];
+      af[ks] = *(const short8*)&s_a[cn*136 + ks*32 + q*8];
     float ps[4] = {0.f,0.f,0.f,0.f}, ps2[4] = {0.f,0.f,0.f,0.f};
     #pragma unroll
-    for (int i = 0; i < 4; i++){
-      const int n0 = (nh*4 + i) * 16;
+    for (int i = 0; i < 2; i++){
+      const int n0 = (w*2 + i) * 16;
       short8 bf[4];
       #pragma unroll
       for (int ks = 0; ks < 4; ks++)
@@ -754,7 +748,7 @@
       #pragma unroll
       for (int r = 0; r < 4; r++){
         float xv = acc[r] + bias;
-        s_x[(m0 + q*4 + r)*130 + n0 + cn] = xv;
+        s_x[(q*4 + r)*130 + n0 + cn] = xv;
         ps[r] += xv; ps2[r] = fmaf(xv, xv, ps2[r]);
       }
     }
@@ -765,18 +759,20 @@
       s += __shfl_xor(s, 2, 64); s2 += __shfl_xor(s2, 2, 64);
       s += __shfl_xor(s, 4, 64); s2 += __shfl_xor(s2, 4, 64);
       s += __shfl_xor(s, 8, 64); s2 += __shfl_xor(s2, 8, 64);
-      if (cn == 0) s_st[(m0 + q*4 + r)*2 + nh] = make_float2(s, s2);
-    }
-  }
-  __syncthreads();
-
-  {
+      if (cn == 0) s_st[(q*4 + r)*4 + w] = make_float2(s, s2);
+    }
+  }
+  __syncthreads();
+
+  {
+    const int d = tid & 127, half = tid >> 7;
     float g = pg[d], c0v = pbb[d];
     #pragma unroll
-    for (int tt = 0; tt < 16; tt++){
-      const int t = half*16 + tt;
-      float2 p0 = s_st[t*2 + 0], p1 = s_st[t*2 + 1];
-      float ssum = p0.x + p1.x, ss2 = p0.y + p1.y;
+    for (int tt = 0; tt < 8; tt++){
+      const int t = half*8 + tt;
+      float2 p0 = s_st[t*4+0], p1 = s_st[t*4+1];
+      float2 p2 = s_st[t*4+2], p3 = s_st[t*4+3];
+      float ssum = p0.x+p1.x+p2.x+p3.x, ss2 = p0.y+p1.y+p2.y+p3.y;
       float mu = ssum * (1.f/128.f);
       float rs = rsqrtf(ss2 * (1.f/128.f) - mu*mu + 1e-5f);
       float v = (s_x[t*130 + d] - mu) * rs * g + c0v;
@@ -785,12 +781,12 @@
   }
   __syncthreads();
 
-  {
+  if (w < 2){
     short8 af[4];
     #pragma unroll
     for (int ks = 0; ks < 4; ks++)
-      af[ks] = *(const short8*)&s_a[(m0 + cn)*136 + ks*32 + q*8];
-    const int n0 = (w >> 1) * 16;
+      af[ks] = *(const short8*)&s_a[cn*136 + ks*32 + q*8];
+    const int n0 = w * 16;
     short8 bf[4];
     #pragma unroll
     for (int ks = 0; ks < 4; ks++)
@@ -803,7 +799,7 @@
       float bias = pb2[col];
       #pragma unroll
       for (int r = 0; r < 4; r++)
-        out[(segtok + m0 + q*4 + r)*NAD + col] = acc[r] + bias;
+        out[(segtok + q*4 + r)*NAD + col] = acc[r] + bias;
     }
   }
 }
@@ -889,7 +885,7 @@
   add(pol_w2, PW2B,  19, 128, 128, 0,  32);
 
   k_prep<<<20*4, 256, 0, stream>>>(P);
-  k_enc12p<<<NTOK/32, 256, 0, stream>>>(obs, W1B, enc_b1, enc_g1, enc_bb1,
+  k_enc12p<<<NTOK/16, 256, 0, stream>>>(obs, W1B, enc_b1, enc_g1, enc_bb1,
       W2B, enc_b2, enc_g2, enc_bb2,
       emb, pact, PWB, proj_b, proj_g, proj_bb, X,
       m_ln_g, m_ln_b, WIGB, WDBCB, m_b_dt,
@@ -897,7 +893,7 @@
       m_a_log, HLA, PPA);
 
   const int carrygrid = BB*1024/256;
-  const int scangrid  = NTOK/32;
+  const int scangrid  = NTOK/16;
 
   k_carry<<<carrygrid, 256, 0, stream>>>(HLA, PPA, h0);
   k_scan2p<<<scangrid, 256, 0, stream>>>(DTb, XINb, Zb, BTu, CTu,
```

Result: no change. 401.3 us (-1.4%).
